# Optimization experiments

Measured on AMD Instinct MI355X. Metric: run time of the kernel, lower is better.

## Reference

```python
import jax, jax.numpy as jnp
import numpy as np

N = 40000
IN_DIM = 2000
HID = 512
OUT_DIM = 30
E = 400000


def setup_inputs() -> dict:
    key = jax.random.key(0)
    k1, k2, k3, k4, k5, k6 = jax.random.split(key, 6)
    features = jax.random.normal(k1, (N, IN_DIM), dtype=jnp.float32)
    edge_index = jax.random.randint(k2, (2, E), 0, N, dtype=jnp.int64)
    # xavier_normal_(gain=1.414): std = gain * sqrt(2/(fan_in+fan_out))
    W1 = jax.random.normal(k3, (IN_DIM, HID), dtype=jnp.float32) * (1.414 * np.sqrt(2.0 / (IN_DIM + HID)))
    W2 = jax.random.normal(k4, (HID, OUT_DIM), dtype=jnp.float32) * (1.414 * np.sqrt(2.0 / (HID + OUT_DIM)))
    att_src = jax.random.normal(k5, (HID,), dtype=jnp.float32) * (1.414 * np.sqrt(2.0 / (1 + HID)))
    att_dst = jax.random.normal(k6, (HID,), dtype=jnp.float32) * (1.414 * np.sqrt(2.0 / (1 + HID)))
    return {"features": features, "W1": W1, "W2": W2,
            "att_src": att_src, "att_dst": att_dst, "edge_index": edge_index}


def _gat_propagate(x_proj, alpha_src, alpha_dst, src, dst, n_nodes):
    """GATConv message+aggregate (heads=1, aggr='add').
    x_proj: [N, C] projected features; alpha_src/alpha_dst: [N] per-node scores.
    """
    score = jax.nn.sigmoid(alpha_src[src] + alpha_dst[dst])          # [E]
    # segment softmax over destination neighborhoods (PyG softmax)
    seg_max = jax.ops.segment_max(score, dst, num_segments=n_nodes)  # [N]
    e = jnp.exp(score - seg_max[dst])                                # [E]
    seg_sum = jax.ops.segment_sum(e, dst, num_segments=n_nodes)     # [N]
    alpha = e / (seg_sum[dst] + 1e-16)                               # [E]
    msg = x_proj[src] * alpha[:, None]                               # [E, C] gather + scale
    return jax.ops.segment_sum(msg, dst, num_segments=n_nodes)      # [N, C] scatter-add


def _stagate_forward(features, W1, W2, att_src, att_dst, src, dst):
    n = features.shape[0]
    # conv1: attention=True (computes its own alpha)
    x1 = features @ W1                                # [N, HID]
    a_src = x1 @ att_src                              # [N]
    a_dst = x1 @ att_dst                              # [N]
    h1 = jax.nn.elu(_gat_propagate(x1, a_src, a_dst, src, dst, n))
    # conv2: attention=False -> just linear projection (heads=1 mean)
    h2 = h1 @ W2                                      # [N, OUT_DIM]
    # conv3: weights tied to W2^T, attention tied to conv1's alphas
    x3 = h2 @ W2.T                                    # [N, HID]
    h3 = jax.nn.elu(_gat_propagate(x3, a_src, a_dst, src, dst, n))
    # conv4: attention=False, weights tied to W1^T
    h4 = h3 @ W1.T                                    # [N, IN_DIM]
    return h2, h4


def reference(features, W1, W2, att_src, att_dst, edge_index):
    src = edge_index[0]
    dst = edge_index[1]
    return _stagate_forward(features, W1, W2, att_src, att_dst, src, dst)
```

## Files before the change

### kernel.cpp

```cpp
#include <hip/hip_runtime.h>
#include <cstdint>

#define NNODES 40000
#define INDIM 2000
#define HIDD 512
#define ODIM 30
#define NEDGES 400000
#define KPAD 2048
#define ROWSPLIT 20224

typedef short bf16x8 __attribute__((ext_vector_type(8)));
typedef float f32x4 __attribute__((ext_vector_type(4)));

__device__ __forceinline__ float bf2f(ushort u){ union{unsigned int i; float f;} x; x.i = ((unsigned int)u)<<16; return x.f; }
__device__ __forceinline__ ushort f2bf(float v){ union{float f; unsigned int u;} x; x.f=v; unsigned int r = x.u + 0x7fffu + ((x.u>>16)&1u); return (ushort)(r>>16); }

__device__ __forceinline__ int xcd_swz(int orig, int nwg){
  int q = nwg >> 3, r = nwg & 7;
  int xcd = orig & 7;
  int idx = orig >> 3;
  return (xcd < r ? xcd*(q+1) : r*(q+1) + (xcd-r)*q) + idx;
}

#define P_MID  asm volatile("" ::: "memory"); __builtin_amdgcn_s_barrier(); \
               asm volatile("s_waitcnt lgkmcnt(0)" ::: "memory"); \
               __builtin_amdgcn_sched_barrier(0); __builtin_amdgcn_s_setprio(1);
#define P_END  __builtin_amdgcn_s_setprio(0); asm volatile("" ::: "memory"); \
               __builtin_amdgcn_s_barrier(); __builtin_amdgcn_sched_barrier(0);
#define P_ENDW __builtin_amdgcn_s_setprio(0); \
               asm volatile("s_waitcnt vmcnt(4)" ::: "memory"); \
               asm volatile("" ::: "memory"); __builtin_amdgcn_s_barrier(); \
               __builtin_amdgcn_sched_barrier(0);

template<typename OutT>
__device__ __forceinline__ void gemm_body(
    const ushort* __restrict__ A, const ushort* __restrict__ Bt,
    OutT* __restrict__ C, int M, int N, int K, int ldc,
    int row0, int col0, char* smem)
{
  ushort* Al = (ushort*)smem;
  ushort* Bl = (ushort*)(smem + 65536);
  const int tid = threadIdx.x;
  const int lane = tid & 63;
  const int w = tid >> 6;
  const int wm = w >> 2, wn = w & 3;
  const int NT = K >> 6;

  f32x4 acc[8][4] = {};
  bf16x8 a[4][2], b[4][2];

  auto stage = [&](bool isA, int kt, int h){
    const ushort* G = isA ? A : Bt;
    int base = isA ? row0 : col0;
    int lim  = isA ? M : N;
    ushort* L = (isA ? Al : Bl) + ((kt & 1) << 14);
    if (kt >= NT) kt -= NT;
    #pragma unroll
    for (int it = 0; it < 2; ++it){
      int ch = tid + (it << 9);
      int rl = (h << 7) + (ch >> 3);
      int cs = ch & 7;
      int gr = base + rl; gr = gr < lim ? gr : lim - 1;
      int gc = (kt << 6) + ((cs ^ (rl & 7)) << 3);
      __builtin_amdgcn_global_load_lds(
        (const __attribute__((address_space(1))) unsigned int*)(G + (size_t)gr*K + gc),
        (__attribute__((address_space(3))) unsigned int*)(L + rl*64 + cs*8), 16, 0, 0);
    }
  };
  auto lda = [&](int buf, int mf, int kk) -> bf16x8 {
    int rl = wm*128 + mf*16 + (lane & 15);
    int ko = kk*32 + ((lane >> 4) << 3);
    return *(const bf16x8*)&Al[(buf << 14) + rl*64 + (ko ^ ((rl & 7) << 3))];
  };
  auto ldb = [&](int buf, int nf, int kk) -> bf16x8 {
    int rl = wn*64 + nf*16 + (lane & 15);
    int ko = kk*32 + ((lane >> 4) << 3);
    return *(const bf16x8*)&Bl[(buf << 14) + rl*64 + (ko ^ ((rl & 7) << 3))];
  };
  auto mfma_q = [&](int mbase, int nbase){
    #pragma unroll
    for (int i=0;i<4;++i)
      #pragma unroll
      for (int j=0;j<2;++j)
        #pragma unroll
        for (int kk=0;kk<2;++kk)
          acc[mbase+i][nbase+j] = __builtin_amdgcn_mfma_f32_16x16x32_bf16(
              a[i][kk], b[nbase+j][kk], acc[mbase+i][nbase+j], 0, 0, 0);
  };

  stage(false, 0, 0); stage(false, 0, 1);
  stage(true , 0, 0); stage(true , 0, 1);
  stage(false, 1, 0); stage(false, 1, 1);
  asm volatile("s_waitcnt vmcnt(4)" ::: "memory");
  asm volatile("" ::: "memory");
  __builtin_amdgcn_s_barrier();
  __builtin_amdgcn_sched_barrier(0);

  const int NT2 = NT >> 1;
  for (int t = 0; t < NT2; ++t){
    const int kt0 = 2*t, kt1 = 2*t + 1;
    #pragma unroll
    for (int i=0;i<4;++i){ a[i][0]=lda(0,i,0); a[i][1]=lda(0,i,1); }
    #pragma unroll
    for (int j=0;j<2;++j){ b[j][0]=ldb(0,j,0); b[j][1]=ldb(0,j,1); }
    stage(true, kt1, 0);
    P_MID; mfma_q(0,0); P_END;
    #pragma unroll
    for (int j=2;j<4;++j){ b[j][0]=ldb(0,j,0); b[j][1]=ldb(0,j,1); }
    stage(true, kt1, 1);
    P_MID; mfma_q(0,2); P_END;
    #pragma unroll
    for (int i=0;i<4;++i){ a[i][0]=lda(0,4+i,0); a[i][1]=lda(0,4+i,1); }
    stage(false, kt0+2, 0);
    P_MID; mfma_q(4,0); P_END;
    stage(false, kt0+2, 1);
    P_MID; mfma_q(4,2); P_ENDW;
    #pragma unroll
    for (int i=0;i<4;++i){ a[i][0]=lda(1,i,0); a[i][1]=lda(1,i,1); }
    #pragma unroll
    for (int j=0;j<2;++j){ b[j][0]=ldb(1,j,0); b[j][1]=ldb(1,j,1); }
    stage(true, kt0+2, 0);
    P_MID; mfma_q(0,0); P_END;
    #pragma unroll
    for (int j=2;j<4;++j){ b[j][0]=ldb(1,j,0); b[j][1]=ldb(1,j,1); }
    stage(true, kt0+2, 1);
    P_MID; mfma_q(0,2); P_END;
    #pragma unroll
    for (int i=0;i<4;++i){ a[i][0]=lda(1,4+i,0); a[i][1]=lda(1,4+i,1); }
    stage(false, kt1+2, 0);
    P_MID; mfma_q(4,0); P_END;
    stage(false, kt1+2, 1);
    P_MID; mfma_q(4,2); P_ENDW;
  }

  asm volatile("s_waitcnt vmcnt(0)" ::: "memory");
  __syncthreads();

  if constexpr (sizeof(OutT)==2) {
    ushort* cs = (ushort*)smem;
    #pragma unroll
    for (int p=0;p<2;++p){
      if (wm == p){
        #pragma unroll
        for (int mf=0;mf<8;++mf)
          #pragma unroll
          for (int nf=0;nf<4;++nf)
            #pragma unroll
            for (int reg=0;reg<4;++reg)
              cs[(mf*16 + ((lane>>4)<<2) + reg)*264 + wn*64 + nf*16 + (lane&15)] = f2bf(acc[mf][nf][reg]);
      }
      __syncthreads();
      #pragma unroll
      for (int it=0; it<8; ++it){
        int ch = tid + it*512;
        int r = ch >> 5, c8 = (ch & 31) * 8;
        int gr = row0 + p*128 + r;
        if (gr < M && col0 + c8 + 8 <= N)
          *(bf16x8*)&((ushort*)C)[(size_t)gr*ldc + col0 + c8] = *(const bf16x8*)&cs[r*264 + c8];
      }
      __syncthreads();
    }
  } else {
    float* cf = (float*)smem;
    #pragma unroll
    for (int p=0;p<4;++p){
      if (wm == (p>>1)){
        int mh = (p & 1) * 4;
        #pragma unroll
        for (int i=0;i<4;++i)
          #pragma unroll
          for (int nf=0;nf<4;++nf)
            #pragma unroll
            for (int reg=0;reg<4;++reg)
              cf[(i*16 + ((lane>>4)<<2) + reg)*260 + wn*64 + nf*16 + (lane&15)] = acc[mh+i][nf][reg];
      }
      __syncthreads();
      #pragma unroll
      for (int it=0; it<8; ++it){
        int ch = tid + it*512;
        int r = ch >> 6, c4 = (ch & 63) * 4;
        int gr = row0 + p*64 + r, gc = col0 + c4;
        if (gr < M && gc + 4 <= N)
          *(f32x4*)&((float*)C)[(size_t)gr*ldc + gc] = *(const f32x4*)&cf[r*260 + c4];
      }
      __syncthreads();
    }
  }
}

__device__ __forceinline__ void cast_rows2(const float* __restrict__ features,
    ushort* __restrict__ featb, int row_base, int cb){
  int t = threadIdx.x;
  int row = row_base + (cb<<1) + (t>>8);
  int kc = t & 255;
  bf16x8 o;
  if (kc < INDIM/8) {
    const float* p = features + (size_t)row*INDIM + kc*8;
    #pragma unroll
    for (int j=0;j<8;++j) o[j] = (short)f2bf(p[j]);
  } else {
    #pragma unroll
    for (int j=0;j<8;++j) o[j] = 0;
  }
  *(bf16x8*)(featb + (size_t)row*KPAD + kc*8) = o;
}

__device__ __forceinline__ void scan_body(const int* __restrict__ degp,
    int* __restrict__ row_ptr, int* part){
  const int t = threadIdx.x;
  const int base = t * 80;
  int s = 0;
  for (int j=0;j<80;++j){ int i = base+j; s += (i < NNODES) ? degp[i] : 0; }
  part[t] = s;
  __syncthreads();
  for (int off=1; off<512; off<<=1){
    int x = (t >= off) ? part[t-off] : 0;
    __syncthreads();
    part[t] += x;
    __syncthreads();
  }
  int run = (t > 0) ? part[t-1] : 0;
  for (int j=0;j<80;++j){
    int i = base+j;
    if (i <= NNODES){
      row_ptr[i] = run;
      if (i < NNODES) run += degp[i];
    }
  }
}

#define S1_CAST   10112
#define S1_W1     (S1_CAST + 2000)
#define S1_W2     (S1_W1 + 32)
#define S1_HIST   (S1_W2 + 782)
#define S1_PAD    (S1_HIST + 48)
#define S1_CUR    (S1_PAD + 79)

__global__ __launch_bounds__(512) void setup_kernel(
    const float* __restrict__ features, const float* __restrict__ W1, const float* __restrict__ W2,
    const int* __restrict__ edst,
    ushort* __restrict__ featb, ushort* __restrict__ W1b, ushort* __restrict__ W1t,
    ushort* __restrict__ W2p, ushort* __restrict__ W2tc,
    int* __restrict__ deg, int* __restrict__ cursor){
  int b = blockIdx.x, t = threadIdx.x;
  if (b < S1_CAST){
    cast_rows2(features, featb, 0, b);
  } else if (b < S1_W1){
    int idx = (b - S1_CAST)*512 + t;
    int r = idx >> 9, c = idx & 511;
    ushort bb = f2bf(W1[idx]);
    W1b[idx] = bb;
    W1t[(size_t)c*KPAD + r] = bb;
  } else if (b < S1_W2){
    int idx = (b - S1_W1)*512 + t;
    int k = idx >> 5, c = idx & 31;
    float val = (c < ODIM) ? W2[k*ODIM + c] : 0.f;
    ushort bb = f2bf(val);
    W2p[k*32 + c] = bb;
    W2tc[c*HIDD + k] = bb;
  } else if (b < S1_HIST){
    int e = (b - S1_W2)*512 + t;
    if (e < NEDGES) atomicAdd(&deg[edst[e]], 1);
  } else if (b < S1_PAD){
    int z = (b - S1_HIST)*512 + t;
    int c = z / 48, r = 2000 + (z - c*48);
    W1t[(size_t)c*KPAD + r] = 0;
  } else {
    int z = (b - S1_PAD)*512 + t;
    if (z < NNODES) cursor[z] = 0;
  }
}

#define K2_G 158
__global__ __launch_bounds__(512, 2) void gemm1a_kernel(
    const ushort* __restrict__ featb, const ushort* __restrict__ W1t, ushort* __restrict__ x1,
    const float* __restrict__ features, ushort* __restrict__ featb_w,
    const int* __restrict__ deg, int* __restrict__ row_ptr){
  __shared__ __align__(16) char smem[131072];
  int b = blockIdx.x;
  if (b < K2_G){
    int s = xcd_swz(b, K2_G);
    int row0 = (s >> 1) << 8;
    int col0 = (s & 1) << 8;
    gemm_body<ushort>(featb, W1t, x1, NNODES, HIDD, KPAD, HIDD, row0, col0, smem);
  } else if (b == K2_G){
    scan_body(deg, row_ptr, (int*)smem);
  } else {
    cast_rows2(features, featb_w, ROWSPLIT, b - K2_G - 1);
  }
}

#define K3_G 156
#define K3_PL (K3_G + 782)
__global__ __launch_bounds__(512, 2) void gemm1b_kernel(
    const ushort* __restrict__ featb, const ushort* __restrict__ W1t, ushort* __restrict__ x1,
    const int* __restrict__ esrc, const int* __restrict__ edst,
    const int* __restrict__ row_ptr, int* __restrict__ cursor, int* __restrict__ csr_src,
    const float* __restrict__ att_src, const float* __restrict__ att_dst,
    float* __restrict__ a_src, float* __restrict__ a_dst){
  __shared__ __align__(16) char smem[131072];
  int b = blockIdx.x, t = threadIdx.x;
  if (b < K3_G){
    int s = xcd_swz(b, K3_G);
    int row0 = ROWSPLIT + ((s >> 1) << 8);
    int col0 = (s & 1) << 8;
    gemm_body<ushort>(featb, W1t, x1, NNODES, HIDD, KPAD, HIDD, row0, col0, smem);
  } else if (b < K3_PL){
    int e = (b - K3_G)*512 + t;
    if (e < NEDGES){
      int d = edst[e];
      int pos = row_ptr[d] + atomicAdd(&cursor[d], 1);
      csr_src[pos] = esrc[e];
    }
  } else {
    int gid = (b - K3_PL)*512 + t;
    int row = gid >> 6, lane = gid & 63;
    bf16x8 v = *(const bf16x8*)(x1 + (size_t)row*HIDD + lane*8);
    float ps = 0.f, pd = 0.f;
    #pragma unroll
    for (int j=0;j<8;++j){
      float xv = bf2f((ushort)v[j]);
      ps += xv * att_src[lane*8+j];
      pd += xv * att_dst[lane*8+j];
    }
    #pragma unroll
    for (int off=32; off>0; off>>=1){ ps += __shfl_down(ps, off); pd += __shfl_down(pd, off); }
    if (lane == 0){ a_src[row] = ps; a_dst[row] = pd; }
  }
}

__global__ __launch_bounds__(512) void a2_kernel(const ushort* __restrict__ x1,
    const float* __restrict__ att_src, const float* __restrict__ att_dst,
    float* __restrict__ a_src, float* __restrict__ a_dst){
  int gid = blockIdx.x*512 + threadIdx.x;
  int row = ROWSPLIT + (gid >> 6), lane = gid & 63;
  if (row >= NNODES) return;
  bf16x8 v = *(const bf16x8*)(x1 + (size_t)row*HIDD + lane*8);
  float ps = 0.f, pd = 0.f;
  #pragma unroll
  for (int j=0;j<8;++j){
    float xv = bf2f((ushort)v[j]);
    ps += xv * att_src[lane*8+j];
    pd += xv * att_dst[lane*8+j];
  }
  #pragma unroll
  for (int off=32; off>0; off>>=1){ ps += __shfl_down(ps, off); pd += __shfl_down(pd, off); }
  if (lane == 0){ a_src[row] = ps; a_dst[row] = pd; }
}

template<typename OutT>
__global__ __launch_bounds__(512, 2) void gemm8_kernel(
    const ushort* __restrict__ A, const ushort* __restrict__ Bt,
    OutT* __restrict__ C, int M, int N, int K, int ldc, int nwg, int cshift)
{
  __shared__ __align__(16) char smem[131072];
  int s = xcd_swz(blockIdx.x, nwg);
  int row0 = (s >> cshift) << 8;
  int col0 = (s & ((1 << cshift) - 1)) << 8;
  gemm_body<OutT>(A, Bt, C, M, N, K, ldc, row0, col0, smem);
}

__global__ __launch_bounds__(256) void agg1_kernel(const ushort* __restrict__ X,
    const int* __restrict__ row_ptr, const int* __restrict__ csr_src,
    const float* __restrict__ a_src, const float* __restrict__ a_dst,
    float* __restrict__ csr_alpha, ushort* __restrict__ outb){
  int gid = blockIdx.x*256 + threadIdx.x;
  int v = gid >> 6, lane = gid & 63;
  if (v >= NNODES) return;
  int p0 = row_ptr[v], p1 = row_ptr[v+1], deg = p1 - p0;
  float ad = a_dst[v];
  float acc[8] = {0.f,0.f,0.f,0.f,0.f,0.f,0.f,0.f};

  if (deg > 0 && deg <= 64){
    bool act = lane < deg;
    int sv = act ? csr_src[p0 + lane] : 0;
    float sc = act ? 1.f/(1.f + __expf(-(a_src[sv] + ad))) : -1e30f;
    float m = sc;
    #pragma unroll
    for (int off=32; off>0; off>>=1) m = fmaxf(m, __shfl_xor(m, off));
    float e = act ? __expf(sc - m) : 0.f;
    float S = e;
    #pragma unroll
    for (int off=32; off>0; off>>=1) S += __shfl_xor(S, off);
    float al = e / (S + 1e-16f);
    if (act) csr_alpha[p0 + lane] = al;
    for (int j=0;j<deg;++j){
      float aj = __shfl(al, j);
      int sj = __shfl(sv, j);
      bf16x8 xv = *(const bf16x8*)(X + (size_t)sj*HIDD + lane*8);
      #pragma unroll
      for (int k=0;k<8;++k) acc[k] += aj * bf2f((ushort)xv[k]);
    }
  } else if (deg > 64){
    float m = -1e30f;
    for (int p = p0 + lane; p < p1; p += 64){
      float sc = 1.f/(1.f + __expf(-(a_src[csr_src[p]] + ad)));
      m = fmaxf(m, sc);
    }
    #pragma unroll
    for (int off=32; off>0; off>>=1) m = fmaxf(m, __shfl_xor(m, off));
    float S = 0.f;
    for (int p = p0 + lane; p < p1; p += 64){
      float sc = 1.f/(1.f + __expf(-(a_src[csr_src[p]] + ad)));
      S += __expf(sc - m);
    }
    #pragma unroll
    for (int off=32; off>0; off>>=1) S += __shfl_xor(S, off);
    float inv = 1.f/(S + 1e-16f);
    for (int base = p0; base < p1; base += 64){
      int p = base + lane;
      bool act = p < p1;
      int sv = act ? csr_src[p] : 0;
      float al = act ? __expf(1.f/(1.f + __expf(-(a_src[sv] + ad))) - m) * inv : 0.f;
      if (act) csr_alpha[p] = al;
      int cnt = p1 - base; cnt = cnt < 64 ? cnt : 64;
      for (int j=0;j<cnt;++j){
        float aj = __shfl(al, j);
        int sj = __shfl(sv, j);
        bf16x8 xv = *(const bf16x8*)(X + (size_t)sj*HIDD + lane*8);
        #pragma unroll
        for (int k=0;k<8;++k) acc[k] += aj * bf2f((ushort)xv[k]);
      }
    }
  }
  bf16x8 o;
  #pragma unroll
  for (int k=0;k<8;++k){
    float a = acc[k];
    a = a > 0.f ? a : __expf(a)-1.f;
    o[k] = (short)f2bf(a);
  }
  *(bf16x8*)(outb + (size_t)v*HIDD + lane*8) = o;
}

__global__ __launch_bounds__(256) void mid_kernel(const ushort* __restrict__ h1,
    const ushort* __restrict__ W2tc, float* __restrict__ h2){
  __shared__ ushort h1s[32*512];
  __shared__ ushort w2s[32*512];
  const int t = threadIdx.x;
  const int row0 = blockIdx.x * 32;
  const ushort* g = h1 + (size_t)row0*HIDD;
  #pragma unroll
  for (int it=0; it<8; ++it){
    int ch = t + it*256;
    *(bf16x8*)&h1s[ch*8] = *(const bf16x8*)&g[ch*8];
    *(bf16x8*)&w2s[ch*8] = *(const bf16x8*)&W2tc[ch*8];
  }
  __syncthreads();
  int c = t & 31, rg = t >> 5;
  if (c < ODIM){
    float acc[4] = {0.f,0.f,0.f,0.f};
    for (int k0=0;k0<64;++k0){
      bf16x8 wv = *(const bf16x8*)&w2s[c*512 + k0*8];
      #pragma unroll
      for (int rr=0; rr<4; ++rr){
        bf16x8 hv = *(const bf16x8*)&h1s[(rg*4+rr)*HIDD + k0*8];
        #pragma unroll
        for (int j=0;j<8;++j) acc[rr] += bf2f((ushort)hv[j]) * bf2f((ushort)wv[j]);
      }
    }
    #pragma unroll
    for (int rr=0;rr<4;++rr) h2[(size_t)(row0 + rg*4 + rr)*ODIM + c] = acc[rr];
  }
}

__global__ __launch_bounds__(256) void conv3_kernel(const float* __restrict__ h2,
    const int* __restrict__ row_ptr, const int* __restrict__ csr_src,
    const float* __restrict__ csr_alpha, const ushort* __restrict__ W2p,
    ushort* __restrict__ h3){
  int gid = blockIdx.x*256 + threadIdx.x;
  int v = gid >> 6, lane = gid & 63;
  if (v >= NNODES) return;
  int p0 = row_ptr[v], p1 = row_ptr[v+1];
  float accd = 0.f;
  if (lane < ODIM){
    for (int p = p0; p < p1; ++p)
      accd += csr_alpha[p] * h2[(size_t)csr_src[p]*ODIM + lane];
  }
  float gv[ODIM];
  #pragma unroll
  for (int ci=0; ci<ODIM; ++ci) gv[ci] = __shfl(accd, ci);
  #pragma unroll
  for (int it=0; it<8; ++it){
    int n = it*64 + lane;
    const ushort* wr = W2p + n*32;
    bf16x8 wvv[4];
    #pragma unroll
    for (int q=0;q<4;++q) wvv[q] = *(const bf16x8*)(wr + q*8);
    float acc = 0.f;
    #pragma unroll
    for (int ci=0; ci<ODIM; ++ci) acc += gv[ci]*bf2f((ushort)wvv[ci>>3][ci&7]);
    acc = acc > 0.f ? acc : __expf(acc)-1.f;
    h3[(size_t)v*HIDD + n] = f2bf(acc);
  }
}

extern "C" void kernel_launch(void* const* d_in, const int* in_sizes, int n_in,
                              void* d_out, int out_size, void* d_ws, size_t ws_size,
                              hipStream_t stream){
  const float* features = (const float*)d_in[0];
  const float* W1 = (const float*)d_in[1];
  const float* W2 = (const float*)d_in[2];
  const float* att_src = (const float*)d_in[3];
  const float* att_dst = (const float*)d_in[4];
  const int* edge = (const int*)d_in[5];
  const int* esrc = edge;
  const int* edst = edge + NEDGES;

  float* h2 = (float*)d_out;
  float* h4 = h2 + (size_t)NNODES*ODIM;
  char* obase = (char*)h4;
  ushort* featb = (ushort*)obase;
  ushort* x1b   = (ushort*)(obase + 163840000);
  ushort* h1b   = (ushort*)(obase + 204800000);

  char* wbase = (char*)d_ws;
  size_t o = 0;
  auto walloc = [&](size_t bytes)->void*{ void* p = wbase + o; o += (bytes + 255) & ~(size_t)255; return p; };
  ushort* h3b      = (ushort*)walloc((size_t)NNODES*HIDD*2);
  ushort* W1b      = (ushort*)walloc((size_t)INDIM*HIDD*2);
  ushort* W1t      = (ushort*)walloc((size_t)HIDD*KPAD*2);
  ushort* W2p      = (ushort*)walloc(512*32*2);
  ushort* W2tc     = (ushort*)walloc(32*512*2);
  float*  a_src    = (float*)walloc(NNODES*4);
  float*  a_dst    = (float*)walloc(NNODES*4);
  int*    deg      = (int*)walloc(NNODES*4);
  int*    cursor   = (int*)walloc(NNODES*4);
  int*    row_ptr  = (int*)walloc((NNODES+1)*4);
  int*    csr_src  = (int*)walloc(NEDGES*4);
  float*  csr_alpha= (float*)walloc(NEDGES*4);

  hipMemsetAsync(deg, 0, NNODES*4, stream);

  setup_kernel<<<S1_CUR, 512, 0, stream>>>(features, W1, W2, edst,
      featb, W1b, W1t, W2p, W2tc, deg, cursor);

  gemm1a_kernel<<<K2_G + 1 + 9888, 512, 0, stream>>>(featb, W1t, x1b,
      features, featb, deg, row_ptr);

  gemm1b_kernel<<<K3_PL + 2528, 512, 0, stream>>>(featb, W1t, x1b,
      esrc, edst, row_ptr, cursor, csr_src, att_src, att_dst, a_src, a_dst);

  a2_kernel<<<2472, 512, 0, stream>>>(x1b, att_src, att_dst, a_src, a_dst);

  agg1_kernel<<<10000, 256, 0, stream>>>(x1b, row_ptr, csr_src, a_src, a_dst, csr_alpha, h1b);
  mid_kernel<<<NNODES/32, 256, 0, stream>>>(h1b, W2tc, h2);
  conv3_kernel<<<10000, 256, 0, stream>>>(h2, row_ptr, csr_src, csr_alpha, W2p, h3b);
  gemm8_kernel<float><<<1256, 512, 0, stream>>>(h3b, W1b, h4,
      NNODES, INDIM, HIDD, INDIM, 1256, 3);
}
```

Measured before the change: 620.4 us.

## Split conv3 and overlap second half with first-half output GEMM, nontemporal stores

Splits conv3 into two row halves: the first half runs alone, then one fused launch runs the h4 GEMM on the first ROWSPLIT rows while other blocks compute conv3 for the remaining rows. A final GEMM launch handles the second row half. This mirrors the existing gemm1a/gemm1b split and is meant to hide the memory-bound conv3 tail under GEMM compute. GEMM output stores also become nontemporal to avoid polluting cache with the large h4 output. It adds a launch and depends on the heterogeneous block mix scheduling well.

Measured after the change: 640.1 us. +3.2%, slower.

```diff
diff --git a/kernel.cpp b/kernel.cpp
--- a/kernel.cpp
+++ b/kernel.cpp
@@ -181,7 +181,8 @@
         int r = ch >> 6, c4 = (ch & 63) * 4;
         int gr = row0 + p*64 + r, gc = col0 + c4;
         if (gr < M && gc + 4 <= N)
-          *(f32x4*)&((float*)C)[(size_t)gr*ldc + gc] = *(const f32x4*)&cf[r*260 + c4];
+          __builtin_nontemporal_store(*(const f32x4*)&cf[r*260 + c4],
+                                      (f32x4*)&((float*)C)[(size_t)gr*ldc + gc]);
       }
       __syncthreads();
     }
@@ -226,6 +227,34 @@
       row_ptr[i] = run;
       if (i < NNODES) run += degp[i];
     }
+  }
+}
+
+__device__ __forceinline__ void conv3_node(int v, int lane,
+    const float* __restrict__ h2, const int* __restrict__ row_ptr,
+    const int* __restrict__ csr_src, const float* __restrict__ csr_alpha,
+    const ushort* __restrict__ W2p, ushort* __restrict__ h3){
+  int p0 = row_ptr[v], p1 = row_ptr[v+1];
+  float accd = 0.f;
+  if (lane < ODIM){
+    for (int p = p0; p < p1; ++p)
+      accd += csr_alpha[p] * h2[(size_t)csr_src[p]*ODIM + lane];
+  }
+  float gv[ODIM];
+  #pragma unroll
+  for (int ci=0; ci<ODIM; ++ci) gv[ci] = __shfl(accd, ci);
+  #pragma unroll
+  for (int it=0; it<8; ++it){
+    int n = it*64 + lane;
+    const ushort* wr = W2p + n*32;
+    bf16x8 wvv[4];
+    #pragma unroll
+    for (int q=0;q<4;++q) wvv[q] = *(const bf16x8*)(wr + q*8);
+    float acc = 0.f;
+    #pragma unroll
+    for (int ci=0; ci<ODIM; ++ci) acc += gv[ci]*bf2f((ushort)wvv[ci>>3][ci&7]);
+    acc = acc > 0.f ? acc : __expf(acc)-1.f;
+    h3[(size_t)v*HIDD + n] = f2bf(acc);
   }
 }
 
@@ -348,18 +377,6 @@
   if (lane == 0){ a_src[row] = ps; a_dst[row] = pd; }
 }
 
-template<typename OutT>
-__global__ __launch_bounds__(512, 2) void gemm8_kernel(
-    const ushort* __restrict__ A, const ushort* __restrict__ Bt,
-    OutT* __restrict__ C, int M, int N, int K, int ldc, int nwg, int cshift)
-{
-  __shared__ __align__(16) char smem[131072];
-  int s = xcd_swz(blockIdx.x, nwg);
-  int row0 = (s >> cshift) << 8;
-  int col0 = (s & ((1 << cshift) - 1)) << 8;
-  gemm_body<OutT>(A, Bt, C, M, N, K, ldc, row0, col0, smem);
-}
-
 __global__ __launch_bounds__(256) void agg1_kernel(const ushort* __restrict__ X,
     const int* __restrict__ row_ptr, const int* __restrict__ csr_src,
     const float* __restrict__ a_src, const float* __restrict__ a_dst,
@@ -464,35 +481,47 @@
   }
 }
 
-__global__ __launch_bounds__(256) void conv3_kernel(const float* __restrict__ h2,
+__global__ __launch_bounds__(256) void conv3a_kernel(const float* __restrict__ h2,
     const int* __restrict__ row_ptr, const int* __restrict__ csr_src,
     const float* __restrict__ csr_alpha, const ushort* __restrict__ W2p,
     ushort* __restrict__ h3){
   int gid = blockIdx.x*256 + threadIdx.x;
   int v = gid >> 6, lane = gid & 63;
-  if (v >= NNODES) return;
-  int p0 = row_ptr[v], p1 = row_ptr[v+1];
-  float accd = 0.f;
-  if (lane < ODIM){
-    for (int p = p0; p < p1; ++p)
-      accd += csr_alpha[p] * h2[(size_t)csr_src[p]*ODIM + lane];
-  }
-  float gv[ODIM];
-  #pragma unroll
-  for (int ci=0; ci<ODIM; ++ci) gv[ci] = __shfl(accd, ci);
-  #pragma unroll
-  for (int it=0; it<8; ++it){
-    int n = it*64 + lane;
-    const ushort* wr = W2p + n*32;
-    bf16x8 wvv[4];
-    #pragma unroll
-    for (int q=0;q<4;++q) wvv[q] = *(const bf16x8*)(wr + q*8);
-    float acc = 0.f;
-    #pragma unroll
-    for (int ci=0; ci<ODIM; ++ci) acc += gv[ci]*bf2f((ushort)wvv[ci>>3][ci&7]);
-    acc = acc > 0.f ? acc : __expf(acc)-1.f;
-    h3[(size_t)v*HIDD + n] = f2bf(acc);
-  }
+  if (v >= ROWSPLIT) return;
+  conv3_node(v, lane, h2, row_ptr, csr_src, csr_alpha, W2p, h3);
+}
+
+#define K9_G 632
+__global__ __launch_bounds__(512, 2) void gemm4a_conv3b_kernel(
+    const ushort* __restrict__ h3b, const ushort* __restrict__ W1b, float* __restrict__ h4,
+    const float* __restrict__ h2, const int* __restrict__ row_ptr,
+    const int* __restrict__ csr_src, const float* __restrict__ csr_alpha,
+    const ushort* __restrict__ W2p, ushort* __restrict__ h3_out){
+  __shared__ __align__(16) char smem[131072];
+  int b = blockIdx.x;
+  if (b < K9_G){
+    int s = xcd_swz(b, K9_G);
+    int row0 = (s >> 3) << 8;
+    int col0 = (s & 7) << 8;
+    gemm_body<float>(h3b, W1b, h4, NNODES, INDIM, HIDD, INDIM, row0, col0, smem);
+  } else {
+    int gid = (b - K9_G)*512 + threadIdx.x;
+    int v = ROWSPLIT + (gid >> 6), lane = gid & 63;
+    if (v >= NNODES) return;
+    conv3_node(v, lane, h2, row_ptr, csr_src, csr_alpha, W2p, h3_out);
+  }
+}
+
+template<typename OutT>
+__global__ __launch_bounds__(512, 2) void gemm8_kernel(
+    const ushort* __restrict__ A, const ushort* __restrict__ Bt,
+    OutT* __restrict__ C, int M, int N, int K, int ldc, int nwg, int cshift, int rowoff)
+{
+  __shared__ __align__(16) char smem[131072];
+  int s = xcd_swz(blockIdx.x, nwg);
+  int row0 = rowoff + ((s >> cshift) << 8);
+  int col0 = (s & ((1 << cshift) - 1)) << 8;
+  gemm_body<OutT>(A, Bt, C, M, N, K, ldc, row0, col0, smem);
 }
 
 extern "C" void kernel_launch(void* const* d_in, const int* in_sizes, int n_in,
@@ -545,7 +574,12 @@
 
   agg1_kernel<<<10000, 256, 0, stream>>>(x1b, row_ptr, csr_src, a_src, a_dst, csr_alpha, h1b);
   mid_kernel<<<NNODES/32, 256, 0, stream>>>(h1b, W2tc, h2);
-  conv3_kernel<<<10000, 256, 0, stream>>>(h2, row_ptr, csr_src, csr_alpha, W2p, h3b);
-  gemm8_kernel<float><<<1256, 512, 0, stream>>>(h3b, W1b, h4,
-      NNODES, INDIM, HIDD, INDIM, 1256, 3);
-}
+
+  conv3a_kernel<<<ROWSPLIT/4, 256, 0, stream>>>(h2, row_ptr, csr_src, csr_alpha, W2p, h3b);
+
+  gemm4a_conv3b_kernel<<<K9_G + 2472, 512, 0, stream>>>(h3b, W1b, h4,
+      h2, row_ptr, csr_src, csr_alpha, W2p, h3b);
+
+  gemm8_kernel<float><<<624, 512, 0, stream>>>(h3b, W1b, h4,
+      NNODES, INDIM, HIDD, INDIM, 624, 3, ROWSPLIT);
+}
```

## Fuse h1 @ W2 projection into agg1 via wave-level transpose-reduce

Applied to the files above, without the earlier changes.

Fold the mid_kernel projection into the aggregation kernel. Each lane applies ELU to its 8 aggregated features, multiplies them by its slice of W2p into 32 partial sums, and reduces across the wave with a butterfly transpose-reduce, so lane c ends up with output column c. This drops the bf16 h1 intermediate write and read, the W2tc transposed copy, and one kernel launch. In exchange agg1 needs about 32 extra accumulator registers and roughly 60 shuffles per node, which could lower occupancy. It also keeps h1 in fp32 rather than rounding it to bf16 before the projection.

Result: slower. 678.9 us (+9.4%).

```diff
diff --git a/kernel.cpp b/kernel.cpp
--- a/kernel.cpp
+++ b/kernel.cpp
@@ -240,7 +240,7 @@
     const float* __restrict__ features, const float* __restrict__ W1, const float* __restrict__ W2,
     const int* __restrict__ edst,
     ushort* __restrict__ featb, ushort* __restrict__ W1b, ushort* __restrict__ W1t,
-    ushort* __restrict__ W2p, ushort* __restrict__ W2tc,
+    ushort* __restrict__ W2p,
     int* __restrict__ deg, int* __restrict__ cursor){
   int b = blockIdx.x, t = threadIdx.x;
   if (b < S1_CAST){
@@ -255,9 +255,7 @@
     int idx = (b - S1_W1)*512 + t;
     int k = idx >> 5, c = idx & 31;
     float val = (c < ODIM) ? W2[k*ODIM + c] : 0.f;
-    ushort bb = f2bf(val);
-    W2p[k*32 + c] = bb;
-    W2tc[c*HIDD + k] = bb;
+    W2p[k*32 + c] = f2bf(val);
   } else if (b < S1_HIST){
     int e = (b - S1_W2)*512 + t;
     if (e < NEDGES) atomicAdd(&deg[edst[e]], 1);
@@ -348,22 +346,11 @@
   if (lane == 0){ a_src[row] = ps; a_dst[row] = pd; }
 }
 
-template<typename OutT>
-__global__ __launch_bounds__(512, 2) void gemm8_kernel(
-    const ushort* __restrict__ A, const ushort* __restrict__ Bt,
-    OutT* __restrict__ C, int M, int N, int K, int ldc, int nwg, int cshift)
-{
-  __shared__ __align__(16) char smem[131072];
-  int s = xcd_swz(blockIdx.x, nwg);
-  int row0 = (s >> cshift) << 8;
-  int col0 = (s & ((1 << cshift) - 1)) << 8;
-  gemm_body<OutT>(A, Bt, C, M, N, K, ldc, row0, col0, smem);
-}
-
 __global__ __launch_bounds__(256) void agg1_kernel(const ushort* __restrict__ X,
     const int* __restrict__ row_ptr, const int* __restrict__ csr_src,
     const float* __restrict__ a_src, const float* __restrict__ a_dst,
-    float* __restrict__ csr_alpha, ushort* __restrict__ outb){
+    const ushort* __restrict__ W2p,
+    float* __restrict__ csr_alpha, float* __restrict__ h2){
   int gid = blockIdx.x*256 + threadIdx.x;
   int v = gid >> 6, lane = gid & 63;
   if (v >= NNODES) return;
@@ -423,45 +410,70 @@
       }
     }
   }
-  bf16x8 o;
+  float hv[8];
   #pragma unroll
   for (int k=0;k<8;++k){
     float a = acc[k];
-    a = a > 0.f ? a : __expf(a)-1.f;
-    o[k] = (short)f2bf(a);
-  }
-  *(bf16x8*)(outb + (size_t)v*HIDD + lane*8) = o;
-}
-
-__global__ __launch_bounds__(256) void mid_kernel(const ushort* __restrict__ h1,
-    const ushort* __restrict__ W2tc, float* __restrict__ h2){
-  __shared__ ushort h1s[32*512];
-  __shared__ ushort w2s[32*512];
-  const int t = threadIdx.x;
-  const int row0 = blockIdx.x * 32;
-  const ushort* g = h1 + (size_t)row0*HIDD;
-  #pragma unroll
-  for (int it=0; it<8; ++it){
-    int ch = t + it*256;
-    *(bf16x8*)&h1s[ch*8] = *(const bf16x8*)&g[ch*8];
-    *(bf16x8*)&w2s[ch*8] = *(const bf16x8*)&W2tc[ch*8];
-  }
-  __syncthreads();
-  int c = t & 31, rg = t >> 5;
-  if (c < ODIM){
-    float acc[4] = {0.f,0.f,0.f,0.f};
-    for (int k0=0;k0<64;++k0){
-      bf16x8 wv = *(const bf16x8*)&w2s[c*512 + k0*8];
-      #pragma unroll
-      for (int rr=0; rr<4; ++rr){
-        bf16x8 hv = *(const bf16x8*)&h1s[(rg*4+rr)*HIDD + k0*8];
-        #pragma unroll
-        for (int j=0;j<8;++j) acc[rr] += bf2f((ushort)hv[j]) * bf2f((ushort)wv[j]);
-      }
-    }
-    #pragma unroll
-    for (int rr=0;rr<4;++rr) h2[(size_t)(row0 + rg*4 + rr)*ODIM + c] = acc[rr];
-  }
+    hv[k] = a > 0.f ? a : __expf(a)-1.f;
+  }
+  float pc[32];
+  #pragma unroll
+  for (int c=0;c<32;++c) pc[c] = 0.f;
+  const ushort* wr = W2p + lane*256;
+  #pragma unroll
+  for (int j=0;j<8;++j){
+    float hj = hv[j];
+    const bf16x8* wrow = (const bf16x8*)(wr + j*32);
+    bf16x8 w0 = wrow[0], w1 = wrow[1], w2v = wrow[2], w3 = wrow[3];
+    #pragma unroll
+    for (int c=0;c<8;++c){
+      pc[c]      += hj * bf2f((ushort)w0[c]);
+      pc[8+c]    += hj * bf2f((ushort)w1[c]);
+      pc[16+c]   += hj * bf2f((ushort)w2v[c]);
+      if (c<6) pc[24+c] += hj * bf2f((ushort)w3[c]);
+    }
+  }
+  #pragma unroll
+  for (int c=0;c<30;++c) pc[c] += __shfl_xor(pc[c], 32);
+  float q[16];
+  { bool up = lane & 1;
+    #pragma unroll
+    for (int i=0;i<16;++i){
+      float a_ = up ? pc[2*i+1] : pc[2*i];
+      float b_ = up ? pc[2*i]   : pc[2*i+1];
+      q[i] = a_ + __shfl_xor(b_, 1);
+    } }
+  float r_[8];
+  { bool up = lane & 2;
+    #pragma unroll
+    for (int i=0;i<8;++i){
+      float a_ = up ? q[2*i+1] : q[2*i];
+      float b_ = up ? q[2*i]   : q[2*i+1];
+      r_[i] = a_ + __shfl_xor(b_, 2);
+    } }
+  float s_[4];
+  { bool up = lane & 4;
+    #pragma unroll
+    for (int i=0;i<4;++i){
+      float a_ = up ? r_[2*i+1] : r_[2*i];
+      float b_ = up ? r_[2*i]   : r_[2*i+1];
+      s_[i] = a_ + __shfl_xor(b_, 4);
+    } }
+  float t_[2];
+  { bool up = lane & 8;
+    #pragma unroll
+    for (int i=0;i<2;++i){
+      float a_ = up ? s_[2*i+1] : s_[2*i];
+      float b_ = up ? s_[2*i]   : s_[2*i+1];
+      t_[i] = a_ + __shfl_xor(b_, 8);
+    } }
+  float u_;
+  { bool up = lane & 16;
+    float a_ = up ? t_[1] : t_[0];
+    float b_ = up ? t_[0] : t_[1];
+    u_ = a_ + __shfl_xor(b_, 16);
+  }
+  if (lane < ODIM) h2[(size_t)v*ODIM + lane] = u_;
 }
 
 __global__ __launch_bounds__(256) void conv3_kernel(const float* __restrict__ h2,
@@ -483,16 +495,28 @@
   #pragma unroll
   for (int it=0; it<8; ++it){
     int n = it*64 + lane;
-    const ushort* wr = W2p + n*32;
+    const ushort* wrp = W2p + n*32;
     bf16x8 wvv[4];
     #pragma unroll
-    for (int q=0;q<4;++q) wvv[q] = *(const bf16x8*)(wr + q*8);
+    for (int qd=0;qd<4;++qd) wvv[qd] = *(const bf16x8*)(wrp + qd*8);
     float acc = 0.f;
     #pragma unroll
     for (int ci=0; ci<ODIM; ++ci) acc += gv[ci]*bf2f((ushort)wvv[ci>>3][ci&7]);
     acc = acc > 0.f ? acc : __expf(acc)-1.f;
     h3[(size_t)v*HIDD + n] = f2bf(acc);
   }
+}
+
+template<typename OutT>
+__global__ __launch_bounds__(512, 2) void gemm8_kernel(
+    const ushort* __restrict__ A, const ushort* __restrict__ Bt,
+    OutT* __restrict__ C, int M, int N, int K, int ldc, int nwg, int cshift)
+{
+  __shared__ __align__(16) char smem[131072];
+  int s = xcd_swz(blockIdx.x, nwg);
+  int row0 = (s >> cshift) << 8;
+  int col0 = (s & ((1 << cshift) - 1)) << 8;
+  gemm_body<OutT>(A, Bt, C, M, N, K, ldc, row0, col0, smem);
 }
 
 extern "C" void kernel_launch(void* const* d_in, const int* in_sizes, int n_in,
@@ -512,7 +536,6 @@
   char* obase = (char*)h4;
   ushort* featb = (ushort*)obase;
   ushort* x1b   = (ushort*)(obase + 163840000);
-  ushort* h1b   = (ushort*)(obase + 204800000);
 
   char* wbase = (char*)d_ws;
   size_t o = 0;
@@ -521,7 +544,6 @@
   ushort* W1b      = (ushort*)walloc((size_t)INDIM*HIDD*2);
   ushort* W1t      = (ushort*)walloc((size_t)HIDD*KPAD*2);
   ushort* W2p      = (ushort*)walloc(512*32*2);
-  ushort* W2tc     = (ushort*)walloc(32*512*2);
   float*  a_src    = (float*)walloc(NNODES*4);
   float*  a_dst    = (float*)walloc(NNODES*4);
   int*    deg      = (int*)walloc(NNODES*4);
@@ -533,7 +555,7 @@
   hipMemsetAsync(deg, 0, NNODES*4, stream);
 
   setup_kernel<<<S1_CUR, 512, 0, stream>>>(features, W1, W2, edst,
-      featb, W1b, W1t, W2p, W2tc, deg, cursor);
+      featb, W1b, W1t, W2p, deg, cursor);
 
   gemm1a_kernel<<<K2_G + 1 + 9888, 512, 0, stream>>>(featb, W1t, x1b,
       features, featb, deg, row_ptr);
@@ -543,9 +565,10 @@
 
   a2_kernel<<<2472, 512, 0, stream>>>(x1b, att_src, att_dst, a_src, a_dst);
 
-  agg1_kernel<<<10000, 256, 0, stream>>>(x1b, row_ptr, csr_src, a_src, a_dst, csr_alpha, h1b);
-  mid_kernel<<<NNODES/32, 256, 0, stream>>>(h1b, W2tc, h2);
+  agg1_kernel<<<10000, 256, 0, stream>>>(x1b, row_ptr, csr_src, a_src, a_dst, W2p, csr_alpha, h2);
+
   conv3_kernel<<<10000, 256, 0, stream>>>(h2, row_ptr, csr_src, csr_alpha, W2p, h3b);
+
   gemm8_kernel<float><<<1256, 512, 0, stream>>>(h3b, W1b, h4,
       NNODES, INDIM, HIDD, INDIM, 1256, 3);
 }
```

## Split edge-softmax into separate kernel and unroll gathers in aggregation kernels

Applied to the files above, without the earlier changes.

Moves the per-destination edge softmax out of agg1 into a new alpha_kernel that uses 16 lanes per node and writes normalized alphas to csr_alpha. agg1 then reads the precomputed alphas and unrolls its neighbor loop by 8 and 4, so several independent row gathers are in flight at once. conv3 gets a similar 4-way unroll. Wave-uniform row pointers are forced into scalar registers. In exchange there is one extra launch and an extra pass that writes and reads the alpha array.

Result: faster. 593.4 us (-4.3%).

```diff
diff --git a/kernel.cpp b/kernel.cpp
--- a/kernel.cpp
+++ b/kernel.cpp
@@ -348,80 +348,75 @@
   if (lane == 0){ a_src[row] = ps; a_dst[row] = pd; }
 }
 
-template<typename OutT>
-__global__ __launch_bounds__(512, 2) void gemm8_kernel(
-    const ushort* __restrict__ A, const ushort* __restrict__ Bt,
-    OutT* __restrict__ C, int M, int N, int K, int ldc, int nwg, int cshift)
-{
-  __shared__ __align__(16) char smem[131072];
-  int s = xcd_swz(blockIdx.x, nwg);
-  int row0 = (s >> cshift) << 8;
-  int col0 = (s & ((1 << cshift) - 1)) << 8;
-  gemm_body<OutT>(A, Bt, C, M, N, K, ldc, row0, col0, smem);
+__global__ __launch_bounds__(256) void alpha_kernel(const int* __restrict__ row_ptr,
+    const int* __restrict__ csr_src, const float* __restrict__ a_src,
+    const float* __restrict__ a_dst, float* __restrict__ csr_alpha){
+  int gid = blockIdx.x*256 + threadIdx.x;
+  int v = gid >> 4, lane = gid & 15;
+  if (v >= NNODES) return;
+  int p0 = row_ptr[v], p1 = row_ptr[v+1];
+  if (p0 >= p1) return;
+  float ad = a_dst[v];
+  float m = -1e30f;
+  for (int p = p0 + lane; p < p1; p += 16){
+    float s = 1.f/(1.f + __expf(-(a_src[csr_src[p]] + ad)));
+    m = fmaxf(m, s);
+  }
+  #pragma unroll
+  for (int off=8; off>0; off>>=1) m = fmaxf(m, __shfl_xor(m, off));
+  float sum = 0.f;
+  for (int p = p0 + lane; p < p1; p += 16){
+    float s = 1.f/(1.f + __expf(-(a_src[csr_src[p]] + ad)));
+    float e = __expf(s - m);
+    csr_alpha[p] = e;
+    sum += e;
+  }
+  #pragma unroll
+  for (int off=8; off>0; off>>=1) sum += __shfl_xor(sum, off);
+  float inv = 1.f/(sum + 1e-16f);
+  for (int p = p0 + lane; p < p1; p += 16) csr_alpha[p] *= inv;
 }
 
 __global__ __launch_bounds__(256) void agg1_kernel(const ushort* __restrict__ X,
     const int* __restrict__ row_ptr, const int* __restrict__ csr_src,
-    const float* __restrict__ a_src, const float* __restrict__ a_dst,
-    float* __restrict__ csr_alpha, ushort* __restrict__ outb){
+    const float* __restrict__ csr_alpha, ushort* __restrict__ outb){
   int gid = blockIdx.x*256 + threadIdx.x;
   int v = gid >> 6, lane = gid & 63;
   if (v >= NNODES) return;
-  int p0 = row_ptr[v], p1 = row_ptr[v+1], deg = p1 - p0;
-  float ad = a_dst[v];
+  int p0 = __builtin_amdgcn_readfirstlane(row_ptr[v]);
+  int p1 = __builtin_amdgcn_readfirstlane(row_ptr[v+1]);
   float acc[8] = {0.f,0.f,0.f,0.f,0.f,0.f,0.f,0.f};
-
-  if (deg > 0 && deg <= 64){
-    bool act = lane < deg;
-    int sv = act ? csr_src[p0 + lane] : 0;
-    float sc = act ? 1.f/(1.f + __expf(-(a_src[sv] + ad))) : -1e30f;
-    float m = sc;
-    #pragma unroll
-    for (int off=32; off>0; off>>=1) m = fmaxf(m, __shfl_xor(m, off));
-    float e = act ? __expf(sc - m) : 0.f;
-    float S = e;
-    #pragma unroll
-    for (int off=32; off>0; off>>=1) S += __shfl_xor(S, off);
-    float al = e / (S + 1e-16f);
-    if (act) csr_alpha[p0 + lane] = al;
-    for (int j=0;j<deg;++j){
-      float aj = __shfl(al, j);
-      int sj = __shfl(sv, j);
-      bf16x8 xv = *(const bf16x8*)(X + (size_t)sj*HIDD + lane*8);
+  int p = p0;
+  for (; p + 8 <= p1; p += 8){
+    int s[8]; float A[8];
+    #pragma unroll
+    for (int u=0;u<8;++u){ s[u] = csr_src[p+u]; A[u] = csr_alpha[p+u]; }
+    bf16x8 x[8];
+    #pragma unroll
+    for (int u=0;u<8;++u) x[u] = *(const bf16x8*)(X + (size_t)s[u]*HIDD + lane*8);
+    #pragma unroll
+    for (int u=0;u<8;++u)
       #pragma unroll
-      for (int k=0;k<8;++k) acc[k] += aj * bf2f((ushort)xv[k]);
-    }
-  } else if (deg > 64){
-    float m = -1e30f;
-    for (int p = p0 + lane; p < p1; p += 64){
-      float sc = 1.f/(1.f + __expf(-(a_src[csr_src[p]] + ad)));
-      m = fmaxf(m, sc);
-    }
-    #pragma unroll
-    for (int off=32; off>0; off>>=1) m = fmaxf(m, __shfl_xor(m, off));
-    float S = 0.f;
-    for (int p = p0 + lane; p < p1; p += 64){
-      float sc = 1.f/(1.f + __expf(-(a_src[csr_src[p]] + ad)));
-      S += __expf(sc - m);
-    }
-    #pragma unroll
-    for (int off=32; off>0; off>>=1) S += __shfl_xor(S, off);
-    float inv = 1.f/(S + 1e-16f);
-    for (int base = p0; base < p1; base += 64){
-      int p = base + lane;
-      bool act = p < p1;
-      int sv = act ? csr_src[p] : 0;
-      float al = act ? __expf(1.f/(1.f + __expf(-(a_src[sv] + ad))) - m) * inv : 0.f;
-      if (act) csr_alpha[p] = al;
-      int cnt = p1 - base; cnt = cnt < 64 ? cnt : 64;
-      for (int j=0;j<cnt;++j){
-        float aj = __shfl(al, j);
-        int sj = __shfl(sv, j);
-        bf16x8 xv = *(const bf16x8*)(X + (size_t)sj*HIDD + lane*8);
-        #pragma unroll
-        for (int k=0;k<8;++k) acc[k] += aj * bf2f((ushort)xv[k]);
-      }
-    }
+      for (int k=0;k<8;++k) acc[k] += A[u] * bf2f((ushort)x[u][k]);
+  }
+  for (; p + 4 <= p1; p += 4){
+    int s0 = csr_src[p], s1 = csr_src[p+1], s2 = csr_src[p+2], s3 = csr_src[p+3];
+    float A0 = csr_alpha[p], A1 = csr_alpha[p+1], A2 = csr_alpha[p+2], A3 = csr_alpha[p+3];
+    bf16x8 x0 = *(const bf16x8*)(X + (size_t)s0*HIDD + lane*8);
+    bf16x8 x1 = *(const bf16x8*)(X + (size_t)s1*HIDD + lane*8);
+    bf16x8 x2 = *(const bf16x8*)(X + (size_t)s2*HIDD + lane*8);
+    bf16x8 x3 = *(const bf16x8*)(X + (size_t)s3*HIDD + lane*8);
+    #pragma unroll
+    for (int k=0;k<8;++k)
+      acc[k] += A0*bf2f((ushort)x0[k]) + A1*bf2f((ushort)x1[k])
+              + A2*bf2f((ushort)x2[k]) + A3*bf2f((ushort)x3[k]);
+  }
+  for (; p < p1; ++p){
+    int sj = csr_src[p];
+    float aj = csr_alpha[p];
+    bf16x8 xv = *(const bf16x8*)(X + (size_t)sj*HIDD + lane*8);
+    #pragma unroll
+    for (int k=0;k<8;++k) acc[k] += aj * bf2f((ushort)xv[k]);
   }
   bf16x8 o;
   #pragma unroll
@@ -471,10 +466,18 @@
   int gid = blockIdx.x*256 + threadIdx.x;
   int v = gid >> 6, lane = gid & 63;
   if (v >= NNODES) return;
-  int p0 = row_ptr[v], p1 = row_ptr[v+1];
+  int p0 = __builtin_amdgcn_readfirstlane(row_ptr[v]);
+  int p1 = __builtin_amdgcn_readfirstlane(row_ptr[v+1]);
   float accd = 0.f;
   if (lane < ODIM){
-    for (int p = p0; p < p1; ++p)
+    int p = p0;
+    for (; p + 4 <= p1; p += 4){
+      int s0 = csr_src[p], s1 = csr_src[p+1], s2 = csr_src[p+2], s3 = csr_src[p+3];
+      float a0 = csr_alpha[p], a1 = csr_alpha[p+1], a2 = csr_alpha[p+2], a3 = csr_alpha[p+3];
+      accd += a0*h2[(size_t)s0*ODIM + lane] + a1*h2[(size_t)s1*ODIM + lane]
+            + a2*h2[(size_t)s2*ODIM + lane] + a3*h2[(size_t)s3*ODIM + lane];
+    }
+    for (; p < p1; ++p)
       accd += csr_alpha[p] * h2[(size_t)csr_src[p]*ODIM + lane];
   }
   float gv[ODIM];
@@ -483,16 +486,28 @@
   #pragma unroll
   for (int it=0; it<8; ++it){
     int n = it*64 + lane;
-    const ushort* wr = W2p + n*32;
+    const ushort* wrp = W2p + n*32;
     bf16x8 wvv[4];
     #pragma unroll
-    for (int q=0;q<4;++q) wvv[q] = *(const bf16x8*)(wr + q*8);
+    for (int qd=0;qd<4;++qd) wvv[qd] = *(const bf16x8*)(wrp + qd*8);
     float acc = 0.f;
     #pragma unroll
     for (int ci=0; ci<ODIM; ++ci) acc += gv[ci]*bf2f((ushort)wvv[ci>>3][ci&7]);
     acc = acc > 0.f ? acc : __expf(acc)-1.f;
     h3[(size_t)v*HIDD + n] = f2bf(acc);
   }
+}
+
+template<typename OutT>
+__global__ __launch_bounds__(512, 2) void gemm8_kernel(
+    const ushort* __restrict__ A, const ushort* __restrict__ Bt,
+    OutT* __restrict__ C, int M, int N, int K, int ldc, int nwg, int cshift)
+{
+  __shared__ __align__(16) char smem[131072];
+  int s = xcd_swz(blockIdx.x, nwg);
+  int row0 = (s >> cshift) << 8;
+  int col0 = (s & ((1 << cshift) - 1)) << 8;
+  gemm_body<OutT>(A, Bt, C, M, N, K, ldc, row0, col0, smem);
 }
 
 extern "C" void kernel_launch(void* const* d_in, const int* in_sizes, int n_in,
@@ -543,7 +558,9 @@
 
   a2_kernel<<<2472, 512, 0, stream>>>(x1b, att_src, att_dst, a_src, a_dst);
 
-  agg1_kernel<<<10000, 256, 0, stream>>>(x1b, row_ptr, csr_src, a_src, a_dst, csr_alpha, h1b);
+  alpha_kernel<<<2500, 256, 0, stream>>>(row_ptr, csr_src, a_src, a_dst, csr_alpha);
+
+  agg1_kernel<<<10000, 256, 0, stream>>>(x1b, row_ptr, csr_src, csr_alpha, h1b);
   mid_kernel<<<NNODES/32, 256, 0, stream>>>(h1b, W2tc, h2);
   conv3_kernel<<<10000, 256, 0, stream>>>(h2, row_ptr, csr_src, csr_alpha, W2p, h3b);
   gemm8_kernel<float><<<1256, 512, 0, stream>>>(h3b, W1b, h4,
```
